# Kernel optimization log

Hardware: AMD Instinct MI355X
Metric: run time of the kernel (lower is better)

The kernel has to match this reference:

```python
import jax, jax.numpy as jnp
import numpy as np

Z_NUM_LIST = [[1,1]]*12 + [[2,1]] + [[2,2]]*11 + [[4,2]] + [[4,4]]*11  # 36 layers
Z_DIM, IN_SZ, OUT_SZ, FS = 64, 16, 16, 3
N_Z = sum(o*i for o, i in Z_NUM_LIST)  # 242
_OFFS = np.concatenate([[0], np.cumsum([o*i for o, i in Z_NUM_LIST])]).astype(int)
BN_EPS = 1e-5


def setup_inputs() -> dict:
    key = jax.random.key(0)
    ks = jax.random.split(key, 8)
    x = jax.random.normal(ks[0], (1024, 3, 32, 32), dtype=jnp.float32)
    conv_w = jax.random.normal(ks[1], (16, 3, 3, 3), dtype=jnp.float32) * 0.1
    conv_b = jnp.zeros((16,), dtype=jnp.float32)
    bn_gamma = jnp.ones((16,), dtype=jnp.float32)
    bn_beta = jnp.zeros((16,), dtype=jnp.float32)
    z_all = jax.random.normal(ks[2], (N_Z, Z_DIM), dtype=jnp.float32)  # 242 z-vectors
    # HyperNet params: z -> (in_sz*z_dim), reshape (in_sz, z_dim), -> (in_sz, out_sz*f*f)
    w2 = jax.random.normal(ks[3], (Z_DIM, IN_SZ * Z_DIM), dtype=jnp.float32) * 0.125
    b2 = jnp.zeros((IN_SZ * Z_DIM,), dtype=jnp.float32)
    w1 = jax.random.normal(ks[4], (Z_DIM, OUT_SZ * FS * FS), dtype=jnp.float32) * 0.125
    b1 = jnp.zeros((OUT_SZ * FS * FS,), dtype=jnp.float32)
    return {"x": x, "conv_w": conv_w, "conv_b": conv_b, "bn_gamma": bn_gamma,
            "bn_beta": bn_beta, "z_all": z_all, "w1": w1, "b1": b1, "w2": w2, "b2": b2}


def _hypernet_batched(z_all, w1, b1, w2, b2):
    # All 242 tiny per-z MLPs as one stacked GEMM pair.
    h_in = (z_all @ w2 + b2).reshape(-1, IN_SZ, Z_DIM)          # [N, 16, 64]
    h_fin = jnp.einsum('nid,do->nio', h_in, w1) + b1            # [N, 16, 144]
    return h_fin.reshape(-1, OUT_SZ, IN_SZ, FS, FS)             # torch .view semantics


def _assemble_weights(kernels):
    # Replicates nested torch.cat(dim=1) then cat(dim=0) per Embedding.
    weights = []
    for li, (o_n, i_n) in enumerate(Z_NUM_LIST):
        k = kernels[_OFFS[li]:_OFFS[li + 1]].reshape(o_n, i_n, OUT_SZ, IN_SZ, FS, FS)
        w = k.transpose(0, 2, 1, 3, 4, 5).reshape(o_n * OUT_SZ, i_n * IN_SZ, FS, FS)
        weights.append(w)
    return weights


def reference(x, conv_w, conv_b, bn_gamma, bn_beta, z_all, w1, b1, w2, b2):
    # conv1 (3->16, 3x3, pad 1)
    y = jax.lax.conv_general_dilated(x, conv_w, (1, 1), 'SAME',
                                     dimension_numbers=('NCHW', 'OIHW', 'NCHW'))
    y = y + conv_b[None, :, None, None]
    # batchnorm (training mode: batch statistics) + relu
    mean = jnp.mean(y, axis=(0, 2, 3))
    var = jnp.var(y, axis=(0, 2, 3))
    y = (y - mean[None, :, None, None]) * jax.lax.rsqrt(var + BN_EPS)[None, :, None, None]
    y = jax.nn.relu(y * bn_gamma[None, :, None, None] + bn_beta[None, :, None, None])
    # hypernetwork weight generation (36 conv weight tensors)
    kernels = _hypernet_batched(z_all, w1, b1, w2, b2)
    weights = _assemble_weights(kernels)
    return (*weights, y)
```

## Files before the change

### kernel.cpp

```cpp
#include <hip/hip_runtime.h>

#define N_Z     242
#define W_ELEMS (N_Z * 2304)
#define NHW_F   1048576.0f

__constant__ int c_offs[37] = {0,1,2,3,4,5,6,7,8,9,10,11,12,14,18,22,26,30,34,38,
                               42,46,50,54,58,66,82,98,114,130,146,162,178,194,210,226,242};
__constant__ int c_isz[36] = {1,1,1,1,1,1,1,1,1,1,1,1, 1, 2,2,2,2,2,2,2,2,2,2,2, 2,
                              4,4,4,4,4,4,4,4,4,4,4};

template<int CTRL, int RMASK>
__device__ __forceinline__ float dpp_add(float x) {
    int s = __builtin_amdgcn_update_dpp(0, __float_as_int(x), CTRL, RMASK, 0xF, true);
    return x + __int_as_float(s);
}
__device__ __forceinline__ float wave_sum64(float x) {
    x = dpp_add<0x111, 0xF>(x);
    x = dpp_add<0x112, 0xF>(x);
    x = dpp_add<0x114, 0xF>(x);
    x = dpp_add<0x118, 0xF>(x);
    x = dpp_add<0x142, 0xA>(x);
    x = dpp_add<0x143, 0xC>(x);
    return x;
}

__device__ __forceinline__ void load_window_g(const float* __restrict__ xp,
                                              float xv[3][3][6], int h, int w0)
{
    #pragma unroll
    for (int ci = 0; ci < 3; ++ci)
        #pragma unroll
        for (int rr = 0; rr < 3; ++rr) {
            const int row  = h + rr - 1;
            const int rowc = min(31, max(0, row));
            const float* rowp = xp + ci * 1024 + rowc * 32;
            const float4 m = *(const float4*)(rowp + w0);
            const float  l = (w0 > 0)  ? rowp[w0 - 1] : 0.0f;
            const float  r = (w0 < 28) ? rowp[w0 + 4] : 0.0f;
            const bool   vr = ((unsigned)row < 32u);
            xv[ci][rr][0] = vr ? l   : 0.0f;
            xv[ci][rr][1] = vr ? m.x : 0.0f;
            xv[ci][rr][2] = vr ? m.y : 0.0f;
            xv[ci][rr][3] = vr ? m.z : 0.0f;
            xv[ci][rr][4] = vr ? m.w : 0.0f;
            xv[ci][rr][5] = vr ? r   : 0.0f;
        }
}

template<typename F>
__device__ __forceinline__ void conv16(const float xv[3][3][6],
                                       const float* __restrict__ cb,
                                       const float* __restrict__ cw,
                                       F&& body)
{
    #pragma unroll
    for (int co = 0; co < 16; ++co) {
        const float bias = cb[co];
        float a0 = bias, a1 = bias, a2 = bias, a3 = bias;
        #pragma unroll
        for (int ci = 0; ci < 3; ++ci)
            #pragma unroll
            for (int rr = 0; rr < 3; ++rr) {
                const float wA = cw[co * 27 + ci * 9 + rr * 3 + 0];
                const float wB = cw[co * 27 + ci * 9 + rr * 3 + 1];
                const float wC = cw[co * 27 + ci * 9 + rr * 3 + 2];
                a0 += wA * xv[ci][rr][0] + wB * xv[ci][rr][1] + wC * xv[ci][rr][2];
                a1 += wA * xv[ci][rr][1] + wB * xv[ci][rr][2] + wC * xv[ci][rr][3];
                a2 += wA * xv[ci][rr][2] + wB * xv[ci][rr][3] + wC * xv[ci][rr][4];
                a3 += wA * xv[ci][rr][3] + wB * xv[ci][rr][4] + wC * xv[ci][rr][5];
            }
        body(co, a0, a1, a2, a3);
    }
}

union Smem1 {
    struct { float zsh[64]; float hin[1024]; } h;
    struct { float red[4][32]; } c;
};

__global__ __launch_bounds__(256, 4) void fused_hyper_stats(
    const float* __restrict__ x,     const float* __restrict__ cw,
    const float* __restrict__ cb,
    const float* __restrict__ z_all, const float* __restrict__ w1,
    const float* __restrict__ b1,    const float* __restrict__ w2,
    const float* __restrict__ b2,    float* __restrict__ out,
    float* __restrict__ gacc)
{
    __shared__ Smem1 sm;
    const int t = threadIdx.x;

    if (blockIdx.x < N_Z) {
        const int n = blockIdx.x;
        if (t < 64) sm.h.zsh[t] = z_all[n * 64 + t];
        __syncthreads();
        float4 a = *(const float4*)(b2 + 4 * t);
        for (int e = 0; e < 64; ++e) {
            const float zv = sm.h.zsh[e];
            const float4 wr = *(const float4*)(w2 + e * 1024 + 4 * t);
            a.x += zv * wr.x; a.y += zv * wr.y; a.z += zv * wr.z; a.w += zv * wr.w;
        }
        *(float4*)(sm.h.hin + 4 * t) = a;
        __syncthreads();

        int li = 0;
        while (n >= c_offs[li + 1]) ++li;
        const int r   = n - c_offs[li];
        const int isz = c_isz[li];
        const int sh  = isz >> 1;
        const int o   = r >> sh;
        const int ii  = r & (isz - 1);
        float* wout = out + (long)c_offs[li] * 2304;

        const int aI = t >> 4, q = t & 15;
        float acc[9];
        #pragma unroll
        for (int j = 0; j < 9; ++j) acc[j] = b1[9 * q + j];
        const float* hp = sm.h.hin + aI * 64;
        const float* wp = w1 + 9 * q;
        #pragma unroll 4
        for (int d = 0; d < 64; ++d) {
            const float hv = hp[d];
            #pragma unroll
            for (int j = 0; j < 9; ++j) acc[j] += hv * wp[d * 144 + j];
        }
        float* op = wout + (o * 16 + aI) * (isz * 144) + (ii * 16 + q) * 9;
        #pragma unroll
        for (int j = 0; j < 9; ++j) op[j] = acc[j];
    } else {
        const int n = blockIdx.x - N_Z;
        const float* xp = x + n * 3072;
        const int h = t >> 3, w0 = (t & 7) << 2;
        float xv[3][3][6];
        load_window_g(xp, xv, h, w0);

        const int lane = t & 63, wid = t >> 6;
        conv16(xv, cb, cw, [&](int co, float a0, float a1, float a2, float a3) {
            float s  = wave_sum64(a0 + a1 + a2 + a3);
            float qv = wave_sum64(a0 * a0 + a1 * a1 + a2 * a2 + a3 * a3);
            if (lane == 63) { sm.c.red[wid][co] = s; sm.c.red[wid][16 + co] = qv; }
        });
        __syncthreads();
        if (t < 32) {
            const float v = sm.c.red[0][t] + sm.c.red[1][t] +
                            sm.c.red[2][t] + sm.c.red[3][t];
            atomicAdd(&gacc[(n & 7) * 32 + t], v);
        }
    }
}

__global__ __launch_bounds__(256, 4) void conv_bn_relu_kernel(
    const float* __restrict__ x,    const float* __restrict__ cw,
    const float* __restrict__ cb,   const float* __restrict__ gacc,
    const float* __restrict__ gamma,const float* __restrict__ beta,
    float* __restrict__ y)
{
    __shared__ float ssh[32];
    const int n = blockIdx.x, t = threadIdx.x;

    if (t < 16) {
        float S = 0.0f, Q = 0.0f;
        #pragma unroll
        for (int k = 0; k < 8; ++k) {
            S += gacc[k * 32 + t];
            Q += gacc[k * 32 + 16 + t];
        }
        const float inv  = 1.0f / NHW_F;
        const float mean = S * inv;
        const float var  = Q * inv - mean * mean;
        const float rs   = rsqrtf(var + 1e-5f);
        const float sc   = gamma[t] * rs;
        ssh[2 * t]     = sc;
        ssh[2 * t + 1] = beta[t] - mean * sc;
    }

    const float* xp = x + n * 3072;
    const int h = t >> 3, w0 = (t & 7) << 2;
    float xv[3][3][6];
    load_window_g(xp, xv, h, w0);
    __syncthreads();

    float* yp = y + n * 16384;
    conv16(xv, cb, cw, [&](int co, float a0, float a1, float a2, float a3) {
        const float sc = ssh[2 * co], sf = ssh[2 * co + 1];
        float4 o4;
        o4.x = fmaxf(0.0f, a0 * sc + sf);
        o4.y = fmaxf(0.0f, a1 * sc + sf);
        o4.z = fmaxf(0.0f, a2 * sc + sf);
        o4.w = fmaxf(0.0f, a3 * sc + sf);
        *(float4*)(yp + co * 1024 + h * 32 + w0) = o4;
    });
}

extern "C" void kernel_launch(void* const* d_in, const int* in_sizes, int n_in,
                              void* d_out, int out_size, void* d_ws, size_t ws_size,
                              hipStream_t stream)
{
    const float* x     = (const float*)d_in[0];
    const float* cw    = (const float*)d_in[1];
    const float* cb    = (const float*)d_in[2];
    const float* gamma = (const float*)d_in[3];
    const float* beta  = (const float*)d_in[4];
    const float* z_all = (const float*)d_in[5];
    const float* w1    = (const float*)d_in[6];
    const float* b1    = (const float*)d_in[7];
    const float* w2    = (const float*)d_in[8];
    const float* b2    = (const float*)d_in[9];

    float* out  = (float*)d_out;
    float* gacc = (float*)d_ws;
    float* y    = out + W_ELEMS;

    fused_hyper_stats<<<N_Z + 1024, 256, 0, stream>>>(x, cw, cb, z_all, w1, b1,
                                                      w2, b2, out, gacc);
    conv_bn_relu_kernel<<<1024, 256, 0, stream>>>(x, cw, cb, gacc, gamma, beta, y);
}
```

Baseline: 131.7 us.

## Split conv work to two outputs per thread and compute BN scale inline

Each image is now handled by two blocks, each thread computing 2 output pixels instead of 4. This doubles the grid and lowers register pressure, and launch bounds are raised to 6 blocks per SM. The BN-apply kernel drops its shared-memory/syncthreads setup and recomputes scale and shift per channel in every thread from gacc. Output is written with nontemporal float2 stores. The cost is redundant conv window loads and more per-thread stats recomputation.

Result: slower. 202.1 us (+53.5%).

```diff
diff --git a/kernel.cpp b/kernel.cpp
--- a/kernel.cpp
+++ b/kernel.cpp
@@ -8,6 +8,9 @@
                                42,46,50,54,58,66,82,98,114,130,146,162,178,194,210,226,242};
 __constant__ int c_isz[36] = {1,1,1,1,1,1,1,1,1,1,1,1, 1, 2,2,2,2,2,2,2,2,2,2,2, 2,
                               4,4,4,4,4,4,4,4,4,4,4};
+
+typedef __attribute__((ext_vector_type(2))) float f2;
+typedef __attribute__((ext_vector_type(4), aligned(4))) float f4u;
 
 template<int CTRL, int RMASK>
 __device__ __forceinline__ float dpp_add(float x) {
@@ -24,9 +27,11 @@
     return x;
 }
 
-__device__ __forceinline__ void load_window_g(const float* __restrict__ xp,
-                                              float xv[3][3][6], int h, int w0)
-{
+__device__ __forceinline__ void load_window2(const float* __restrict__ xp,
+                                             float xv[3][3][4], int h, int w0)
+{
+    const bool e0  = (w0 == 0), e30 = (w0 == 30);
+    const int  off = e0 ? 0 : (e30 ? 28 : (w0 - 1));
     #pragma unroll
     for (int ci = 0; ci < 3; ++ci)
         #pragma unroll
@@ -34,29 +39,29 @@
             const int row  = h + rr - 1;
             const int rowc = min(31, max(0, row));
             const float* rowp = xp + ci * 1024 + rowc * 32;
-            const float4 m = *(const float4*)(rowp + w0);
-            const float  l = (w0 > 0)  ? rowp[w0 - 1] : 0.0f;
-            const float  r = (w0 < 28) ? rowp[w0 + 4] : 0.0f;
-            const bool   vr = ((unsigned)row < 32u);
-            xv[ci][rr][0] = vr ? l   : 0.0f;
-            xv[ci][rr][1] = vr ? m.x : 0.0f;
-            xv[ci][rr][2] = vr ? m.y : 0.0f;
-            xv[ci][rr][3] = vr ? m.z : 0.0f;
-            xv[ci][rr][4] = vr ? m.w : 0.0f;
-            xv[ci][rr][5] = vr ? r   : 0.0f;
+            const f4u g = *(const f4u*)(rowp + off);
+            const bool vr = ((unsigned)row < 32u);
+            const float v0 = e0 ? 0.0f : (e30 ? g.y : g.x);
+            const float v1 = e0 ? g.x  : (e30 ? g.z : g.y);
+            const float v2 = e0 ? g.y  : (e30 ? g.w : g.z);
+            const float v3 = e0 ? g.z  : (e30 ? 0.0f : g.w);
+            xv[ci][rr][0] = vr ? v0 : 0.0f;
+            xv[ci][rr][1] = vr ? v1 : 0.0f;
+            xv[ci][rr][2] = vr ? v2 : 0.0f;
+            xv[ci][rr][3] = vr ? v3 : 0.0f;
         }
 }
 
 template<typename F>
-__device__ __forceinline__ void conv16(const float xv[3][3][6],
-                                       const float* __restrict__ cb,
-                                       const float* __restrict__ cw,
-                                       F&& body)
+__device__ __forceinline__ void conv16_2(const float xv[3][3][4],
+                                         const float* __restrict__ cb,
+                                         const float* __restrict__ cw,
+                                         F&& body)
 {
     #pragma unroll
     for (int co = 0; co < 16; ++co) {
         const float bias = cb[co];
-        float a0 = bias, a1 = bias, a2 = bias, a3 = bias;
+        float a0 = bias, a1 = bias;
         #pragma unroll
         for (int ci = 0; ci < 3; ++ci)
             #pragma unroll
@@ -66,10 +71,8 @@
                 const float wC = cw[co * 27 + ci * 9 + rr * 3 + 2];
                 a0 += wA * xv[ci][rr][0] + wB * xv[ci][rr][1] + wC * xv[ci][rr][2];
                 a1 += wA * xv[ci][rr][1] + wB * xv[ci][rr][2] + wC * xv[ci][rr][3];
-                a2 += wA * xv[ci][rr][2] + wB * xv[ci][rr][3] + wC * xv[ci][rr][4];
-                a3 += wA * xv[ci][rr][3] + wB * xv[ci][rr][4] + wC * xv[ci][rr][5];
             }
-        body(co, a0, a1, a2, a3);
+        body(co, a0, a1);
     }
 }
 
@@ -78,7 +81,7 @@
     struct { float red[4][32]; } c;
 };
 
-__global__ __launch_bounds__(256, 4) void fused_hyper_stats(
+__global__ __launch_bounds__(256, 6) void fused_hyper_stats(
     const float* __restrict__ x,     const float* __restrict__ cw,
     const float* __restrict__ cb,
     const float* __restrict__ z_all, const float* __restrict__ w1,
@@ -127,67 +130,62 @@
         #pragma unroll
         for (int j = 0; j < 9; ++j) op[j] = acc[j];
     } else {
-        const int n = blockIdx.x - N_Z;
+        const int b2i  = blockIdx.x - N_Z;
+        const int n    = b2i >> 1;
+        const int half = b2i & 1;
         const float* xp = x + n * 3072;
-        const int h = t >> 3, w0 = (t & 7) << 2;
-        float xv[3][3][6];
-        load_window_g(xp, xv, h, w0);
+        const int h  = (half << 4) + (t >> 4);
+        const int w0 = (t & 15) << 1;
+        float xv[3][3][4];
+        load_window2(xp, xv, h, w0);
 
         const int lane = t & 63, wid = t >> 6;
-        conv16(xv, cb, cw, [&](int co, float a0, float a1, float a2, float a3) {
-            float s  = wave_sum64(a0 + a1 + a2 + a3);
-            float qv = wave_sum64(a0 * a0 + a1 * a1 + a2 * a2 + a3 * a3);
+        conv16_2(xv, cb, cw, [&](int co, float a0, float a1) {
+            float s  = wave_sum64(a0 + a1);
+            float qv = wave_sum64(a0 * a0 + a1 * a1);
             if (lane == 63) { sm.c.red[wid][co] = s; sm.c.red[wid][16 + co] = qv; }
         });
         __syncthreads();
         if (t < 32) {
             const float v = sm.c.red[0][t] + sm.c.red[1][t] +
                             sm.c.red[2][t] + sm.c.red[3][t];
-            atomicAdd(&gacc[(n & 7) * 32 + t], v);
+            atomicAdd(&gacc[(b2i & 7) * 32 + t], v);
         }
     }
 }
 
-__global__ __launch_bounds__(256, 4) void conv_bn_relu_kernel(
+__global__ __launch_bounds__(256, 6) void conv_bn_relu_kernel(
     const float* __restrict__ x,    const float* __restrict__ cw,
     const float* __restrict__ cb,   const float* __restrict__ gacc,
     const float* __restrict__ gamma,const float* __restrict__ beta,
     float* __restrict__ y)
 {
-    __shared__ float ssh[32];
-    const int n = blockIdx.x, t = threadIdx.x;
-
-    if (t < 16) {
+    const int b = blockIdx.x, t = threadIdx.x;
+    const int n = b >> 1;
+
+    const float* xp = x + n * 3072;
+    const int h  = ((b & 1) << 4) + (t >> 4);
+    const int w0 = (t & 15) << 1;
+    float xv[3][3][4];
+    load_window2(xp, xv, h, w0);
+
+    float* yp = y + n * 16384 + h * 32 + w0;
+    conv16_2(xv, cb, cw, [&](int co, float a0, float a1) {
         float S = 0.0f, Q = 0.0f;
         #pragma unroll
         for (int k = 0; k < 8; ++k) {
-            S += gacc[k * 32 + t];
-            Q += gacc[k * 32 + 16 + t];
+            S += gacc[k * 32 + co];
+            Q += gacc[k * 32 + 16 + co];
         }
         const float inv  = 1.0f / NHW_F;
         const float mean = S * inv;
         const float var  = Q * inv - mean * mean;
-        const float rs   = rsqrtf(var + 1e-5f);
-        const float sc   = gamma[t] * rs;
-        ssh[2 * t]     = sc;
-        ssh[2 * t + 1] = beta[t] - mean * sc;
-    }
-
-    const float* xp = x + n * 3072;
-    const int h = t >> 3, w0 = (t & 7) << 2;
-    float xv[3][3][6];
-    load_window_g(xp, xv, h, w0);
-    __syncthreads();
-
-    float* yp = y + n * 16384;
-    conv16(xv, cb, cw, [&](int co, float a0, float a1, float a2, float a3) {
-        const float sc = ssh[2 * co], sf = ssh[2 * co + 1];
-        float4 o4;
-        o4.x = fmaxf(0.0f, a0 * sc + sf);
-        o4.y = fmaxf(0.0f, a1 * sc + sf);
-        o4.z = fmaxf(0.0f, a2 * sc + sf);
-        o4.w = fmaxf(0.0f, a3 * sc + sf);
-        *(float4*)(yp + co * 1024 + h * 32 + w0) = o4;
+        const float sc   = gamma[co] * rsqrtf(var + 1e-5f);
+        const float sf   = beta[co] - mean * sc;
+        f2 o2;
+        o2.x = fmaxf(0.0f, a0 * sc + sf);
+        o2.y = fmaxf(0.0f, a1 * sc + sf);
+        __builtin_nontemporal_store(o2, (f2*)(yp + co * 1024));
     });
 }
 
@@ -210,7 +208,7 @@
     float* gacc = (float*)d_ws;
     float* y    = out + W_ELEMS;
 
-    fused_hyper_stats<<<N_Z + 1024, 256, 0, stream>>>(x, cw, cb, z_all, w1, b1,
+    fused_hyper_stats<<<N_Z + 2048, 256, 0, stream>>>(x, cw, cb, z_all, w1, b1,
                                                       w2, b2, out, gacc);
-    conv_bn_relu_kernel<<<1024, 256, 0, stream>>>(x, cw, cb, gacc, gamma, beta, y);
-}
+    conv_bn_relu_kernel<<<2048, 256, 0, stream>>>(x, cw, cb, gacc, gamma, beta, y);
+}
```

## Fuse stats, BN-ReLU and hypernet into one cooperative kernel with grid sync

Applied to the files above, without the earlier changes.

Replaces the two-kernel flow with a single cooperative launch of 1024 blocks. Each block computes its conv outputs once and keeps all 16x4 accumulators in registers. It contributes batch statistics via atomics, waits at a grid-wide sync, then applies BN+ReLU and writes y with nontemporal stores. The first 242 blocks then compute the hypernet weights. This removes the second conv recompute, the extra input reread and one launch. The cost is 64 live accumulators per thread, which may raise register pressure, and a grid barrier that requires all 1024 blocks to be co-resident. If the cooperative launch fails, the code falls back to the old two-kernel path.

After: 208.3 us. 1.58x slower.

```diff
diff --git a/kernel.cpp b/kernel.cpp
--- a/kernel.cpp
+++ b/kernel.cpp
@@ -1,4 +1,7 @@
 #include <hip/hip_runtime.h>
+#include <hip/hip_cooperative_groups.h>
+
+namespace cg = cooperative_groups;
 
 #define N_Z     242
 #define W_ELEMS (N_Z * 2304)
@@ -8,6 +11,8 @@
                                42,46,50,54,58,66,82,98,114,130,146,162,178,194,210,226,242};
 __constant__ int c_isz[36] = {1,1,1,1,1,1,1,1,1,1,1,1, 1, 2,2,2,2,2,2,2,2,2,2,2, 2,
                               4,4,4,4,4,4,4,4,4,4,4};
+
+typedef __attribute__((ext_vector_type(4))) float f4n;
 
 template<int CTRL, int RMASK>
 __device__ __forceinline__ float dpp_add(float x) {
@@ -24,27 +29,33 @@
     return x;
 }
 
+__device__ __forceinline__ void load_rows(const float* __restrict__ chbase,
+                                          float xr[3][6], int h, int w0)
+{
+    #pragma unroll
+    for (int rr = 0; rr < 3; ++rr) {
+        const int row  = h + rr - 1;
+        const int rowc = min(31, max(0, row));
+        const float* rowp = chbase + rowc * 32;
+        const float4 m = *(const float4*)(rowp + w0);
+        const float  l = (w0 > 0)  ? rowp[w0 - 1] : 0.0f;
+        const float  r = (w0 < 28) ? rowp[w0 + 4] : 0.0f;
+        const bool   vr = ((unsigned)row < 32u);
+        xr[rr][0] = vr ? l   : 0.0f;
+        xr[rr][1] = vr ? m.x : 0.0f;
+        xr[rr][2] = vr ? m.y : 0.0f;
+        xr[rr][3] = vr ? m.z : 0.0f;
+        xr[rr][4] = vr ? m.w : 0.0f;
+        xr[rr][5] = vr ? r   : 0.0f;
+    }
+}
+
 __device__ __forceinline__ void load_window_g(const float* __restrict__ xp,
                                               float xv[3][3][6], int h, int w0)
 {
     #pragma unroll
     for (int ci = 0; ci < 3; ++ci)
-        #pragma unroll
-        for (int rr = 0; rr < 3; ++rr) {
-            const int row  = h + rr - 1;
-            const int rowc = min(31, max(0, row));
-            const float* rowp = xp + ci * 1024 + rowc * 32;
-            const float4 m = *(const float4*)(rowp + w0);
-            const float  l = (w0 > 0)  ? rowp[w0 - 1] : 0.0f;
-            const float  r = (w0 < 28) ? rowp[w0 + 4] : 0.0f;
-            const bool   vr = ((unsigned)row < 32u);
-            xv[ci][rr][0] = vr ? l   : 0.0f;
-            xv[ci][rr][1] = vr ? m.x : 0.0f;
-            xv[ci][rr][2] = vr ? m.y : 0.0f;
-            xv[ci][rr][3] = vr ? m.z : 0.0f;
-            xv[ci][rr][4] = vr ? m.w : 0.0f;
-            xv[ci][rr][5] = vr ? r   : 0.0f;
-        }
+        load_rows(xp + ci * 1024, xv[ci], h, w0);
 }
 
 template<typename F>
@@ -73,10 +84,146 @@
     }
 }
 
-union Smem1 {
+__device__ __forceinline__ void hypernet_one(int n, int t, float* zsh, float* hin,
+                                             const float* __restrict__ z_all,
+                                             const float* __restrict__ w1,
+                                             const float* __restrict__ b1,
+                                             const float* __restrict__ w2,
+                                             const float* __restrict__ b2,
+                                             float* __restrict__ out)
+{
+    if (t < 64) zsh[t] = z_all[n * 64 + t];
+    __syncthreads();
+    float4 a = *(const float4*)(b2 + 4 * t);
+    for (int e = 0; e < 64; ++e) {
+        const float zv = zsh[e];
+        const float4 wr = *(const float4*)(w2 + e * 1024 + 4 * t);
+        a.x += zv * wr.x; a.y += zv * wr.y; a.z += zv * wr.z; a.w += zv * wr.w;
+    }
+    *(float4*)(hin + 4 * t) = a;
+    __syncthreads();
+
+    int li = 0;
+    while (n >= c_offs[li + 1]) ++li;
+    const int r   = n - c_offs[li];
+    const int isz = c_isz[li];
+    const int sh  = isz >> 1;
+    const int o   = r >> sh;
+    const int ii  = r & (isz - 1);
+    float* wout = out + (long)c_offs[li] * 2304;
+
+    const int aI = t >> 4, q = t & 15;
+    float acc[9];
+    #pragma unroll
+    for (int j = 0; j < 9; ++j) acc[j] = b1[9 * q + j];
+    const float* hp = hin + aI * 64;
+    const float* wp = w1 + 9 * q;
+    #pragma unroll 4
+    for (int d = 0; d < 64; ++d) {
+        const float hv = hp[d];
+        #pragma unroll
+        for (int j = 0; j < 9; ++j) acc[j] += hv * wp[d * 144 + j];
+    }
+    float* op = wout + (o * 16 + aI) * (isz * 144) + (ii * 16 + q) * 9;
+    #pragma unroll
+    for (int j = 0; j < 9; ++j) op[j] = acc[j];
+}
+
+union SmemA {
     struct { float zsh[64]; float hin[1024]; } h;
-    struct { float red[4][32]; } c;
+    struct { float red[4][32]; float ssh[32]; } c;
 };
+
+__global__ __launch_bounds__(256, 4) void fused_all(
+    const float* __restrict__ x,     const float* __restrict__ cw,
+    const float* __restrict__ cb,    const float* __restrict__ gamma,
+    const float* __restrict__ beta,  const float* __restrict__ z_all,
+    const float* __restrict__ w1,    const float* __restrict__ b1,
+    const float* __restrict__ w2,    const float* __restrict__ b2,
+    float* __restrict__ out,         float* __restrict__ gacc,
+    float* __restrict__ y)
+{
+    __shared__ SmemA sm;
+    const int n = blockIdx.x, t = threadIdx.x;
+    const int h = t >> 3, w0 = (t & 7) << 2;
+    const float* xp = x + n * 3072;
+
+    float acc[16][4];
+    #pragma unroll
+    for (int co = 0; co < 16; ++co) {
+        const float b = cb[co];
+        acc[co][0] = b; acc[co][1] = b; acc[co][2] = b; acc[co][3] = b;
+    }
+    #pragma unroll
+    for (int ci = 0; ci < 3; ++ci) {
+        float xr[3][6];
+        load_rows(xp + ci * 1024, xr, h, w0);
+        #pragma unroll
+        for (int co = 0; co < 16; ++co)
+            #pragma unroll
+            for (int rr = 0; rr < 3; ++rr) {
+                const float wA = cw[co * 27 + ci * 9 + rr * 3 + 0];
+                const float wB = cw[co * 27 + ci * 9 + rr * 3 + 1];
+                const float wC = cw[co * 27 + ci * 9 + rr * 3 + 2];
+                acc[co][0] += wA * xr[rr][0] + wB * xr[rr][1] + wC * xr[rr][2];
+                acc[co][1] += wA * xr[rr][1] + wB * xr[rr][2] + wC * xr[rr][3];
+                acc[co][2] += wA * xr[rr][2] + wB * xr[rr][3] + wC * xr[rr][4];
+                acc[co][3] += wA * xr[rr][3] + wB * xr[rr][4] + wC * xr[rr][5];
+            }
+    }
+
+    const int lane = t & 63, wid = t >> 6;
+    #pragma unroll
+    for (int co = 0; co < 16; ++co) {
+        const float s = wave_sum64(acc[co][0] + acc[co][1] + acc[co][2] + acc[co][3]);
+        const float q = wave_sum64(acc[co][0]*acc[co][0] + acc[co][1]*acc[co][1] +
+                                   acc[co][2]*acc[co][2] + acc[co][3]*acc[co][3]);
+        if (lane == 63) { sm.c.red[wid][co] = s; sm.c.red[wid][16 + co] = q; }
+    }
+    __syncthreads();
+    if (t < 32) {
+        const float v = sm.c.red[0][t] + sm.c.red[1][t] +
+                        sm.c.red[2][t] + sm.c.red[3][t];
+        atomicAdd(&gacc[(n & 7) * 32 + t], v);
+    }
+
+    cg::this_grid().sync();
+
+    if (t < 16) {
+        float S = 0.0f, Q = 0.0f;
+        #pragma unroll
+        for (int k = 0; k < 8; ++k) {
+            S += __hip_atomic_load(&gacc[k * 32 + t],
+                                   __ATOMIC_RELAXED, __HIP_MEMORY_SCOPE_AGENT);
+            Q += __hip_atomic_load(&gacc[k * 32 + 16 + t],
+                                   __ATOMIC_RELAXED, __HIP_MEMORY_SCOPE_AGENT);
+        }
+        const float inv  = 1.0f / NHW_F;
+        const float mean = S * inv;
+        const float var  = Q * inv - mean * mean;
+        const float sc   = gamma[t] * rsqrtf(var + 1e-5f);
+        sm.c.ssh[2 * t]     = sc;
+        sm.c.ssh[2 * t + 1] = beta[t] - mean * sc;
+    }
+    __syncthreads();
+
+    float* yp = y + n * 16384 + h * 32 + w0;
+    #pragma unroll
+    for (int co = 0; co < 16; ++co) {
+        const float sc = sm.c.ssh[2 * co], sf = sm.c.ssh[2 * co + 1];
+        f4n o4;
+        o4.x = fmaxf(0.0f, acc[co][0] * sc + sf);
+        o4.y = fmaxf(0.0f, acc[co][1] * sc + sf);
+        o4.z = fmaxf(0.0f, acc[co][2] * sc + sf);
+        o4.w = fmaxf(0.0f, acc[co][3] * sc + sf);
+        __builtin_nontemporal_store(o4, (f4n*)(yp + co * 1024));
+    }
+
+    if (n < N_Z) {
+        __syncthreads();
+        hypernet_one(n, t, sm.h.zsh, sm.h.hin, z_all, w1, b1, w2, b2, out);
+    }
+}
 
 __global__ __launch_bounds__(256, 4) void fused_hyper_stats(
     const float* __restrict__ x,     const float* __restrict__ cw,
@@ -86,46 +233,11 @@
     const float* __restrict__ b2,    float* __restrict__ out,
     float* __restrict__ gacc)
 {
-    __shared__ Smem1 sm;
+    __shared__ SmemA sm;
     const int t = threadIdx.x;
 
     if (blockIdx.x < N_Z) {
-        const int n = blockIdx.x;
-        if (t < 64) sm.h.zsh[t] = z_all[n * 64 + t];
-        __syncthreads();
-        float4 a = *(const float4*)(b2 + 4 * t);
-        for (int e = 0; e < 64; ++e) {
-            const float zv = sm.h.zsh[e];
-            const float4 wr = *(const float4*)(w2 + e * 1024 + 4 * t);
-            a.x += zv * wr.x; a.y += zv * wr.y; a.z += zv * wr.z; a.w += zv * wr.w;
-        }
-        *(float4*)(sm.h.hin + 4 * t) = a;
-        __syncthreads();
-
-        int li = 0;
-        while (n >= c_offs[li + 1]) ++li;
-        const int r   = n - c_offs[li];
-        const int isz = c_isz[li];
-        const int sh  = isz >> 1;
-        const int o   = r >> sh;
-        const int ii  = r & (isz - 1);
-        float* wout = out + (long)c_offs[li] * 2304;
-
-        const int aI = t >> 4, q = t & 15;
-        float acc[9];
-        #pragma unroll
-        for (int j = 0; j < 9; ++j) acc[j] = b1[9 * q + j];
-        const float* hp = sm.h.hin + aI * 64;
-        const float* wp = w1 + 9 * q;
-        #pragma unroll 4
-        for (int d = 0; d < 64; ++d) {
-            const float hv = hp[d];
-            #pragma unroll
-            for (int j = 0; j < 9; ++j) acc[j] += hv * wp[d * 144 + j];
-        }
-        float* op = wout + (o * 16 + aI) * (isz * 144) + (ii * 16 + q) * 9;
-        #pragma unroll
-        for (int j = 0; j < 9; ++j) op[j] = acc[j];
+        hypernet_one(blockIdx.x, t, sm.h.zsh, sm.h.hin, z_all, w1, b1, w2, b2, out);
     } else {
         const int n = blockIdx.x - N_Z;
         const float* xp = x + n * 3072;
@@ -210,7 +322,17 @@
     float* gacc = (float*)d_ws;
     float* y    = out + W_ELEMS;
 
-    fused_hyper_stats<<<N_Z + 1024, 256, 0, stream>>>(x, cw, cb, z_all, w1, b1,
-                                                      w2, b2, out, gacc);
-    conv_bn_relu_kernel<<<1024, 256, 0, stream>>>(x, cw, cb, gacc, gamma, beta, y);
-}
+    void* args[] = { (void*)&x, (void*)&cw, (void*)&cb, (void*)&gamma,
+                     (void*)&beta, (void*)&z_all, (void*)&w1, (void*)&b1,
+                     (void*)&w2, (void*)&b2, (void*)&out, (void*)&gacc,
+                     (void*)&y };
+    hipError_t e = hipLaunchCooperativeKernel((const void*)fused_all,
+                                              dim3(1024), dim3(256),
+                                              args, 0, stream);
+    if (e != hipSuccess) {
+        fused_hyper_stats<<<N_Z + 1024, 256, 0, stream>>>(x, cw, cb, z_all, w1,
+                                                          b1, w2, b2, out, gacc);
+        conv_bn_relu_kernel<<<1024, 256, 0, stream>>>(x, cw, cb, gacc, gamma,
+                                                      beta, y);
+    }
+}
```

## Store conv output in stats pass and apply BN+ReLU in place

Applied to the files above, without the earlier changes.

The stats kernel now writes the raw conv output to y with nontemporal stores while it accumulates batch statistics. The second kernel no longer recomputes the convolution from x. It becomes a streaming elementwise pass that reads y, applies the BN scale/shift and ReLU, and writes it back. This removes the duplicated convolution arithmetic but adds a full extra read and write of the 64 MB activation tensor.

New measurement: 143.1 us. 8.7% more time.

```diff
diff --git a/kernel.cpp b/kernel.cpp
--- a/kernel.cpp
+++ b/kernel.cpp
@@ -8,6 +8,8 @@
                                42,46,50,54,58,66,82,98,114,130,146,162,178,194,210,226,242};
 __constant__ int c_isz[36] = {1,1,1,1,1,1,1,1,1,1,1,1, 1, 2,2,2,2,2,2,2,2,2,2,2, 2,
                               4,4,4,4,4,4,4,4,4,4,4};
+
+typedef __attribute__((ext_vector_type(4))) float f4n;
 
 template<int CTRL, int RMASK>
 __device__ __forceinline__ float dpp_add(float x) {
@@ -73,59 +75,69 @@
     }
 }
 
-union Smem1 {
+__device__ __forceinline__ void hypernet_one(int n, int t, float* zsh, float* hin,
+                                             const float* __restrict__ z_all,
+                                             const float* __restrict__ w1,
+                                             const float* __restrict__ b1,
+                                             const float* __restrict__ w2,
+                                             const float* __restrict__ b2,
+                                             float* __restrict__ out)
+{
+    if (t < 64) zsh[t] = z_all[n * 64 + t];
+    __syncthreads();
+    float4 a = *(const float4*)(b2 + 4 * t);
+    for (int e = 0; e < 64; ++e) {
+        const float zv = zsh[e];
+        const float4 wr = *(const float4*)(w2 + e * 1024 + 4 * t);
+        a.x += zv * wr.x; a.y += zv * wr.y; a.z += zv * wr.z; a.w += zv * wr.w;
+    }
+    *(float4*)(hin + 4 * t) = a;
+    __syncthreads();
+
+    int li = 0;
+    while (n >= c_offs[li + 1]) ++li;
+    const int r   = n - c_offs[li];
+    const int isz = c_isz[li];
+    const int sh  = isz >> 1;
+    const int o   = r >> sh;
+    const int ii  = r & (isz - 1);
+    float* wout = out + (long)c_offs[li] * 2304;
+
+    const int aI = t >> 4, q = t & 15;
+    float acc[9];
+    #pragma unroll
+    for (int j = 0; j < 9; ++j) acc[j] = b1[9 * q + j];
+    const float* hp = hin + aI * 64;
+    const float* wp = w1 + 9 * q;
+    #pragma unroll 4
+    for (int d = 0; d < 64; ++d) {
+        const float hv = hp[d];
+        #pragma unroll
+        for (int j = 0; j < 9; ++j) acc[j] += hv * wp[d * 144 + j];
+    }
+    float* op = wout + (o * 16 + aI) * (isz * 144) + (ii * 16 + q) * 9;
+    #pragma unroll
+    for (int j = 0; j < 9; ++j) op[j] = acc[j];
+}
+
+union SmemA {
     struct { float zsh[64]; float hin[1024]; } h;
     struct { float red[4][32]; } c;
 };
 
-__global__ __launch_bounds__(256, 4) void fused_hyper_stats(
+__global__ __launch_bounds__(256, 4) void fused_hyper_conv(
     const float* __restrict__ x,     const float* __restrict__ cw,
     const float* __restrict__ cb,
     const float* __restrict__ z_all, const float* __restrict__ w1,
     const float* __restrict__ b1,    const float* __restrict__ w2,
     const float* __restrict__ b2,    float* __restrict__ out,
-    float* __restrict__ gacc)
-{
-    __shared__ Smem1 sm;
+    float* __restrict__ gacc,        float* __restrict__ y)
+{
+    __shared__ SmemA sm;
     const int t = threadIdx.x;
 
     if (blockIdx.x < N_Z) {
-        const int n = blockIdx.x;
-        if (t < 64) sm.h.zsh[t] = z_all[n * 64 + t];
-        __syncthreads();
-        float4 a = *(const float4*)(b2 + 4 * t);
-        for (int e = 0; e < 64; ++e) {
-            const float zv = sm.h.zsh[e];
-            const float4 wr = *(const float4*)(w2 + e * 1024 + 4 * t);
-            a.x += zv * wr.x; a.y += zv * wr.y; a.z += zv * wr.z; a.w += zv * wr.w;
-        }
-        *(float4*)(sm.h.hin + 4 * t) = a;
-        __syncthreads();
-
-        int li = 0;
-        while (n >= c_offs[li + 1]) ++li;
-        const int r   = n - c_offs[li];
-        const int isz = c_isz[li];
-        const int sh  = isz >> 1;
-        const int o   = r >> sh;
-        const int ii  = r & (isz - 1);
-        float* wout = out + (long)c_offs[li] * 2304;
-
-        const int aI = t >> 4, q = t & 15;
-        float acc[9];
-        #pragma unroll
-        for (int j = 0; j < 9; ++j) acc[j] = b1[9 * q + j];
-        const float* hp = sm.h.hin + aI * 64;
-        const float* wp = w1 + 9 * q;
-        #pragma unroll 4
-        for (int d = 0; d < 64; ++d) {
-            const float hv = hp[d];
-            #pragma unroll
-            for (int j = 0; j < 9; ++j) acc[j] += hv * wp[d * 144 + j];
-        }
-        float* op = wout + (o * 16 + aI) * (isz * 144) + (ii * 16 + q) * 9;
-        #pragma unroll
-        for (int j = 0; j < 9; ++j) op[j] = acc[j];
+        hypernet_one(blockIdx.x, t, sm.h.zsh, sm.h.hin, z_all, w1, b1, w2, b2, out);
     } else {
         const int n = blockIdx.x - N_Z;
         const float* xp = x + n * 3072;
@@ -133,8 +145,11 @@
         float xv[3][3][6];
         load_window_g(xp, xv, h, w0);
 
+        float* yp = y + n * 16384 + h * 32 + w0;
         const int lane = t & 63, wid = t >> 6;
         conv16(xv, cb, cw, [&](int co, float a0, float a1, float a2, float a3) {
+            f4n o4; o4.x = a0; o4.y = a1; o4.z = a2; o4.w = a3;
+            __builtin_nontemporal_store(o4, (f4n*)(yp + co * 1024));
             float s  = wave_sum64(a0 + a1 + a2 + a3);
             float qv = wave_sum64(a0 * a0 + a1 * a1 + a2 * a2 + a3 * a3);
             if (lane == 63) { sm.c.red[wid][co] = s; sm.c.red[wid][16 + co] = qv; }
@@ -148,14 +163,12 @@
     }
 }
 
-__global__ __launch_bounds__(256, 4) void conv_bn_relu_kernel(
-    const float* __restrict__ x,    const float* __restrict__ cw,
-    const float* __restrict__ cb,   const float* __restrict__ gacc,
-    const float* __restrict__ gamma,const float* __restrict__ beta,
-    float* __restrict__ y)
+__global__ __launch_bounds__(256, 8) void bn_relu_kernel(
+    const float* __restrict__ gacc, const float* __restrict__ gamma,
+    const float* __restrict__ beta, float* __restrict__ y)
 {
     __shared__ float ssh[32];
-    const int n = blockIdx.x, t = threadIdx.x;
+    const int b = blockIdx.x, t = threadIdx.x;
 
     if (t < 16) {
         float S = 0.0f, Q = 0.0f;
@@ -167,28 +180,25 @@
         const float inv  = 1.0f / NHW_F;
         const float mean = S * inv;
         const float var  = Q * inv - mean * mean;
-        const float rs   = rsqrtf(var + 1e-5f);
-        const float sc   = gamma[t] * rs;
+        const float sc   = gamma[t] * rsqrtf(var + 1e-5f);
         ssh[2 * t]     = sc;
         ssh[2 * t + 1] = beta[t] - mean * sc;
     }
-
-    const float* xp = x + n * 3072;
-    const int h = t >> 3, w0 = (t & 7) << 2;
-    float xv[3][3][6];
-    load_window_g(xp, xv, h, w0);
     __syncthreads();
 
-    float* yp = y + n * 16384;
-    conv16(xv, cb, cw, [&](int co, float a0, float a1, float a2, float a3) {
+    float* yp = y + (size_t)b * 8192;
+    #pragma unroll
+    for (int i = 0; i < 8; ++i) {
+        const int idx = (i * 256 + t) * 4;
+        const int co  = ((b & 1) << 3) + i;
         const float sc = ssh[2 * co], sf = ssh[2 * co + 1];
-        float4 o4;
-        o4.x = fmaxf(0.0f, a0 * sc + sf);
-        o4.y = fmaxf(0.0f, a1 * sc + sf);
-        o4.z = fmaxf(0.0f, a2 * sc + sf);
-        o4.w = fmaxf(0.0f, a3 * sc + sf);
-        *(float4*)(yp + co * 1024 + h * 32 + w0) = o4;
-    });
+        f4n v = __builtin_nontemporal_load((const f4n*)(yp + idx));
+        v.x = fmaxf(0.0f, v.x * sc + sf);
+        v.y = fmaxf(0.0f, v.y * sc + sf);
+        v.z = fmaxf(0.0f, v.z * sc + sf);
+        v.w = fmaxf(0.0f, v.w * sc + sf);
+        __builtin_nontemporal_store(v, (f4n*)(yp + idx));
+    }
 }
 
 extern "C" void kernel_launch(void* const* d_in, const int* in_sizes, int n_in,
@@ -210,7 +220,7 @@
     float* gacc = (float*)d_ws;
     float* y    = out + W_ELEMS;
 
-    fused_hyper_stats<<<N_Z + 1024, 256, 0, stream>>>(x, cw, cb, z_all, w1, b1,
-                                                      w2, b2, out, gacc);
-    conv_bn_relu_kernel<<<1024, 256, 0, stream>>>(x, cw, cb, gacc, gamma, beta, y);
-}
+    fused_hyper_conv<<<N_Z + 1024, 256, 0, stream>>>(x, cw, cb, z_all, w1, b1,
+                                                     w2, b2, out, gacc, y);
+    bn_relu_kernel<<<2048, 256, 0, stream>>>(gacc, gamma, beta, y);
+}
```
